# Kernel optimization log

Hardware: AMD Instinct MI355X
Metric: run time of the kernel (lower is better)

Reference implementation:

```python
import jax, jax.numpy as jnp
import numpy as np

B, N, INP = 8, 1024, 7
D, H = 32, 4  # message output dim, attention heads


def setup_inputs() -> dict:
    key = jax.random.key(0)
    ks = jax.random.split(key, 12)
    s = lambda k, shape, fan_in: jax.random.normal(k, shape, jnp.float32) / np.sqrt(fan_in)
    return {
        "x": jax.random.normal(ks[0], (B, N, INP), jnp.float32),
        "W1": s(ks[1], (INP, 64), INP), "b1": jnp.zeros((64,), jnp.float32),
        "W2": s(ks[2], (64, 64), 64),   "b2": jnp.zeros((64,), jnp.float32),
        "W3": s(ks[3], (64, D), 64),    "b3": jnp.zeros((D,), jnp.float32),
        "Wa": s(ks[4], (2 * D, H), 2 * D), "ba": jnp.zeros((H,), jnp.float32),
        "Ws": s(ks[5], (H * D, D), H * D), "bs": jnp.zeros((D,), jnp.float32),
    }


def reference(x, W1, b1, W2, b2, W3, b3, Wa, ba, Ws, bs):
    lrelu = lambda t: jax.nn.leaky_relu(t, 0.2)
    # message MLP: [B,N,INP] -> [B,N,D]
    fx = lrelu(x @ W1 + b1)
    fx = lrelu(fx @ W2 + b2)
    fx = fx @ W3 + b3
    # pairwise score: concat(fx_i, fx_j) @ Wa + ba == fx_i@Wa[:D] + fx_j@Wa[D:] + ba
    s_i = fx @ Wa[:D]   # [B,N,H], contribution of row node i
    s_j = fx @ Wa[D:]   # [B,N,H], contribution of col node j
    score = s_i[:, :, None, :] + s_j[:, None, :, :] + ba  # [B,N,N,H]
    att = jax.nn.softmax(score, axis=2)                    # softmax over j (dim 2)
    # per-head aggregation: out[b,i,h,:] = sum_j att[b,i,j,h] * fx[b,j,:]
    agg = jnp.einsum('bijh,bjd->bihd', att, fx)            # [B,N,H,D]
    att_cat = agg.reshape(B, N, H * D)                     # head-major concat
    return att_cat @ Ws + bs                               # squeeze_back (H>1)
```

## Files before the change

kernel.cpp:

```cpp
#include <hip/hip_runtime.h>


#define BB 8
#define NN 1024
#define TR 32
#define NB1 256

__global__ __launch_bounds__(256) void gat_k1(
    const float* __restrict__ x,
    const float* __restrict__ W1, const float* __restrict__ b1,
    const float* __restrict__ W2, const float* __restrict__ b2,
    const float* __restrict__ W3, const float* __restrict__ b3,
    const float* __restrict__ Wa,
    float* __restrict__ Gp, float* __restrict__ Zp)
{
    const int t   = threadIdx.x;
    const int blk = blockIdx.x;

    __shared__ float W1s[7 * 64];
    __shared__ float W2s[64 * 64];
    __shared__ float W3s[64 * 32];
    __shared__ float Was[32 * 4];
    __shared__ float b1s[64], b2s[64], b3s[32];
    __shared__ float xs[TR * 8];
    __shared__ float h1s[TR * 68];
    __shared__ float h2s[TR * 68];
    __shared__ float fxs[TR * 36];
    __shared__ float es[TR * 4];

    {
        const float4* s2 = (const float4*)W2;
        float4* d2 = (float4*)W2s;
        d2[t] = s2[t]; d2[t + 256] = s2[t + 256];
        d2[t + 512] = s2[t + 512]; d2[t + 768] = s2[t + 768];
        const float4* s3 = (const float4*)W3;
        float4* d3 = (float4*)W3s;
        d3[t] = s3[t]; d3[t + 256] = s3[t + 256];
        if (t < 112) ((float4*)W1s)[t] = ((const float4*)W1)[t];
        if (t < 32)  ((float4*)Was)[t] = ((const float4*)Wa)[32 + t];
        if (t < 16)  ((float4*)b1s)[t] = ((const float4*)b1)[t];
        if (t >= 16 && t < 32) ((float4*)b2s)[t - 16] = ((const float4*)b2)[t - 16];
        if (t >= 32 && t < 40) ((float4*)b3s)[t - 32] = ((const float4*)b3)[t - 32];
        if (t < TR * 7) xs[(t / 7) * 8 + (t % 7)] = x[blk * (TR * 7) + t];
    }
    __syncthreads();

    {
        const int r  = t >> 3;
        const int o0 = (t & 7) * 8;
        float acc[8];
#pragma unroll
        for (int j = 0; j < 8; ++j) acc[j] = b1s[o0 + j];
#pragma unroll
        for (int k = 0; k < 7; ++k) {
            const float xv = xs[r * 8 + k];
#pragma unroll
            for (int j = 0; j < 8; ++j)
                acc[j] = fmaf(xv, W1s[k * 64 + o0 + j], acc[j]);
        }
#pragma unroll
        for (int j = 0; j < 8; ++j)
            h1s[r * 68 + o0 + j] = fmaxf(acc[j], 0.2f * acc[j]);
    }
    __syncthreads();

    {
        const int o0 = (t & 15) * 4;
        const int r0 = (t >> 4) * 2;
        float a0[4], a1[4];
#pragma unroll
        for (int j = 0; j < 4; ++j) { a0[j] = b2s[o0 + j]; a1[j] = b2s[o0 + j]; }
#pragma unroll
        for (int k4 = 0; k4 < 64; k4 += 4) {
            const float4 hA = *(const float4*)&h1s[r0 * 68 + k4];
            const float4 hB = *(const float4*)&h1s[(r0 + 1) * 68 + k4];
            const float ha[4] = {hA.x, hA.y, hA.z, hA.w};
            const float hb[4] = {hB.x, hB.y, hB.z, hB.w};
#pragma unroll
            for (int kk = 0; kk < 4; ++kk) {
                const float4 w = *(const float4*)&W2s[(k4 + kk) * 64 + o0];
                a0[0] = fmaf(ha[kk], w.x, a0[0]); a0[1] = fmaf(ha[kk], w.y, a0[1]);
                a0[2] = fmaf(ha[kk], w.z, a0[2]); a0[3] = fmaf(ha[kk], w.w, a0[3]);
                a1[0] = fmaf(hb[kk], w.x, a1[0]); a1[1] = fmaf(hb[kk], w.y, a1[1]);
                a1[2] = fmaf(hb[kk], w.z, a1[2]); a1[3] = fmaf(hb[kk], w.w, a1[3]);
            }
        }
        *(float4*)&h2s[r0 * 68 + o0] = make_float4(
            fmaxf(a0[0], 0.2f * a0[0]), fmaxf(a0[1], 0.2f * a0[1]),
            fmaxf(a0[2], 0.2f * a0[2]), fmaxf(a0[3], 0.2f * a0[3]));
        *(float4*)&h2s[(r0 + 1) * 68 + o0] = make_float4(
            fmaxf(a1[0], 0.2f * a1[0]), fmaxf(a1[1], 0.2f * a1[1]),
            fmaxf(a1[2], 0.2f * a1[2]), fmaxf(a1[3], 0.2f * a1[3]));
    }
    __syncthreads();

    {
        const int r  = t >> 3;
        const int o0 = (t & 7) * 4;
        float acc[4];
#pragma unroll
        for (int j = 0; j < 4; ++j) acc[j] = b3s[o0 + j];
#pragma unroll
        for (int k4 = 0; k4 < 64; k4 += 4) {
            const float4 hv = *(const float4*)&h2s[r * 68 + k4];
            const float hh[4] = {hv.x, hv.y, hv.z, hv.w};
#pragma unroll
            for (int kk = 0; kk < 4; ++kk) {
                const float4 w = *(const float4*)&W3s[(k4 + kk) * 32 + o0];
                acc[0] = fmaf(hh[kk], w.x, acc[0]); acc[1] = fmaf(hh[kk], w.y, acc[1]);
                acc[2] = fmaf(hh[kk], w.z, acc[2]); acc[3] = fmaf(hh[kk], w.w, acc[3]);
            }
        }
        *(float4*)&fxs[r * 36 + o0] = make_float4(acc[0], acc[1], acc[2], acc[3]);
    }
    __syncthreads();

    if (t < TR * 4) {
        const int r = t >> 2, h = t & 3;
        float s = 0.f;
#pragma unroll 8
        for (int k = 0; k < 32; ++k) s = fmaf(fxs[r * 36 + k], Was[k * 4 + h], s);
        es[r * 4 + h] = __expf(s);
    }
    __syncthreads();

    if (t < 128) {
        const int h = t >> 5, d = t & 31;
        float g = 0.f;
#pragma unroll 8
        for (int r = 0; r < TR; ++r) g = fmaf(es[r * 4 + h], fxs[r * 36 + d], g);
        Gp[blk * 128 + t] = g;
    } else if (t < 132) {
        const int h = t - 128;
        float z = 0.f;
#pragma unroll 8
        for (int r = 0; r < TR; ++r) z += es[r * 4 + h];
        Zp[blk * 4 + h] = z;
    }
}

__global__ __launch_bounds__(256) void gat_k2(
    const float* __restrict__ Gp, const float* __restrict__ Zp,
    const float* __restrict__ Ws, const float* __restrict__ bs,
    float* __restrict__ out)
{
    const int blk   = blockIdx.x;
    const int b     = blk >> 4;
    const int slice = blk & 15;
    const int t     = threadIdx.x;

    __shared__ float Gc[128];
    __shared__ float zsh[4];
    __shared__ float red[8 * 32];
    __shared__ float orow[32];

    float g = 0.f;
    if (t < 128) {
        const float* gp = Gp + (size_t)(b * 32) * 128 + t;
#pragma unroll 8
        for (int i = 0; i < 32; ++i) g += gp[i * 128];
    } else if (t < 132) {
        const int h = t - 128;
        float z = 0.f;
#pragma unroll 8
        for (int i = 0; i < 32; ++i) z += Zp[(b * 32 + i) * 4 + h];
        zsh[h] = z;
    }
    __syncthreads();
    if (t < 128) Gc[t] = g / zsh[t >> 5];
    __syncthreads();

    {
        const int o = t & 31, p = t >> 5;
        float a = (p == 0) ? bs[o] : 0.f;
#pragma unroll
        for (int kk = 0; kk < 16; ++kk) {
            const int k = p * 16 + kk;
            a = fmaf(Gc[k], Ws[k * 32 + o], a);
        }
        red[p * 32 + o] = a;
    }
    __syncthreads();
    if (t < 32) {
        float a = 0.f;
#pragma unroll
        for (int p = 0; p < 8; ++p) a += red[p * 32 + t];
        orow[t] = a;
    }
    __syncthreads();

    const float4 v4 = ((const float4*)orow)[t & 7];
    const int rl = t >> 3;
    const int row0 = slice * 64 + rl;
    ((float4*)out)[((size_t)b * NN + row0) * 8 + (t & 7)] = v4;
    ((float4*)out)[((size_t)b * NN + row0 + 32) * 8 + (t & 7)] = v4;
}

extern "C" void kernel_launch(void* const* d_in, const int* in_sizes, int n_in,
                              void* d_out, int out_size, void* d_ws, size_t ws_size,
                              hipStream_t stream) {
    const float* x  = (const float*)d_in[0];
    const float* W1 = (const float*)d_in[1];
    const float* b1 = (const float*)d_in[2];
    const float* W2 = (const float*)d_in[3];
    const float* b2 = (const float*)d_in[4];
    const float* W3 = (const float*)d_in[5];
    const float* b3 = (const float*)d_in[6];
    const float* Wa = (const float*)d_in[7];
    const float* Ws = (const float*)d_in[9];
    const float* bs = (const float*)d_in[10];
    float* out = (float*)d_out;

    float* Gp = (float*)d_ws;
    float* Zp = Gp + NB1 * 128;

    gat_k1<<<dim3(NB1), dim3(256), 0, stream>>>(
        x, W1, b1, W2, b2, W3, b3, Wa, Gp, Zp);
    gat_k2<<<dim3(128), dim3(256), 0, stream>>>(Gp, Zp, Ws, bs, out);
}
```

Before: 83.70 us.

## Fuse both kernels into one with a grid-wide atomic barrier

Merges the MLP/partial-sum kernel and the reduction/projection kernel into a single launch of 256 blocks. The blocks synchronise through a global atomic counter spin-wait, which is reset with a memset before each launch. After the barrier each block reduces its batch's partials and writes 32 output rows. This removes one kernel launch and the gap between the two kernels, but it adds a memset, a spin barrier that relies on all 256 blocks being co-resident, and redundant per-block reductions.

```diff
diff --git a/kernel.cpp b/kernel.cpp
--- a/kernel.cpp
+++ b/kernel.cpp
@@ -4,15 +4,18 @@
 #define BB 8
 #define NN 1024
 #define TR 32
-#define NB1 256
-
-__global__ __launch_bounds__(256) void gat_k1(
+#define NB 256
+
+__global__ __launch_bounds__(256) void gat_fused(
     const float* __restrict__ x,
     const float* __restrict__ W1, const float* __restrict__ b1,
     const float* __restrict__ W2, const float* __restrict__ b2,
     const float* __restrict__ W3, const float* __restrict__ b3,
     const float* __restrict__ Wa,
-    float* __restrict__ Gp, float* __restrict__ Zp)
+    const float* __restrict__ Ws, const float* __restrict__ bs,
+    float* __restrict__ Gp, float* __restrict__ Zp,
+    unsigned int* __restrict__ ctr,
+    float* __restrict__ out)
 {
     const int t   = threadIdx.x;
     const int blk = blockIdx.x;
@@ -27,6 +30,11 @@
     __shared__ float h2s[TR * 68];
     __shared__ float fxs[TR * 36];
     __shared__ float es[TR * 4];
+    __shared__ float Gsh[128];
+    __shared__ float Gc[128];
+    __shared__ float zsh[4];
+    __shared__ float red[8 * 32];
+    __shared__ float orow[32];
 
     {
         const float4* s2 = (const float4*)W2;
@@ -137,28 +145,27 @@
         for (int r = 0; r < TR; ++r) z += es[r * 4 + h];
         Zp[blk * 4 + h] = z;
     }
-}
-
-__global__ __launch_bounds__(256) void gat_k2(
-    const float* __restrict__ Gp, const float* __restrict__ Zp,
-    const float* __restrict__ Ws, const float* __restrict__ bs,
-    float* __restrict__ out)
-{
-    const int blk   = blockIdx.x;
-    const int b     = blk >> 4;
-    const int slice = blk & 15;
-    const int t     = threadIdx.x;
-
-    __shared__ float Gc[128];
-    __shared__ float zsh[4];
-    __shared__ float red[8 * 32];
-    __shared__ float orow[32];
-
-    float g = 0.f;
+
+    __syncthreads();
+    if (t == 0) {
+        __threadfence();
+        __hip_atomic_fetch_add(ctr, 1u, __ATOMIC_ACQ_REL,
+                               __HIP_MEMORY_SCOPE_AGENT);
+        while (__hip_atomic_load(ctr, __ATOMIC_RELAXED,
+                                 __HIP_MEMORY_SCOPE_AGENT) < NB) { }
+        __threadfence();
+    }
+    __syncthreads();
+
+    const int b     = blk >> 5;
+    const int slice = blk & 31;
+
     if (t < 128) {
         const float* gp = Gp + (size_t)(b * 32) * 128 + t;
+        float g = 0.f;
 #pragma unroll 8
         for (int i = 0; i < 32; ++i) g += gp[i * 128];
+        Gsh[t] = g;
     } else if (t < 132) {
         const int h = t - 128;
         float z = 0.f;
@@ -167,7 +174,7 @@
         zsh[h] = z;
     }
     __syncthreads();
-    if (t < 128) Gc[t] = g / zsh[t >> 5];
+    if (t < 128) Gc[t] = Gsh[t] / zsh[t >> 5];
     __syncthreads();
 
     {
@@ -189,11 +196,11 @@
     }
     __syncthreads();
 
-    const float4 v4 = ((const float4*)orow)[t & 7];
-    const int rl = t >> 3;
-    const int row0 = slice * 64 + rl;
-    ((float4*)out)[((size_t)b * NN + row0) * 8 + (t & 7)] = v4;
-    ((float4*)out)[((size_t)b * NN + row0 + 32) * 8 + (t & 7)] = v4;
+    {
+        const int row = slice * 32 + (t >> 3);
+        ((float4*)out)[((size_t)b * NN + row) * 8 + (t & 7)] =
+            ((const float4*)orow)[t & 7];
+    }
 }
 
 extern "C" void kernel_launch(void* const* d_in, const int* in_sizes, int n_in,
@@ -211,10 +218,11 @@
     const float* bs = (const float*)d_in[10];
     float* out = (float*)d_out;
 
-    float* Gp = (float*)d_ws;
-    float* Zp = Gp + NB1 * 128;
-
-    gat_k1<<<dim3(NB1), dim3(256), 0, stream>>>(
-        x, W1, b1, W2, b2, W3, b3, Wa, Gp, Zp);
-    gat_k2<<<dim3(128), dim3(256), 0, stream>>>(Gp, Zp, Ws, bs, out);
+    unsigned int* ctr = (unsigned int*)d_ws;
+    float* Gp = (float*)d_ws + 64;
+    float* Zp = Gp + NB * 128;
+
+    hipMemsetAsync(ctr, 0, sizeof(unsigned int), stream);
+    gat_fused<<<dim3(NB), dim3(256), 0, stream>>>(
+        x, W1, b1, W2, b2, W3, b3, Wa, Ws, bs, Gp, Zp, ctr, out);
 }
```

New measurement: 98.37 us. +17.5%, slower.
